# Kernel tuning notes

Hardware: AMD Instinct MI355X
Metric: run time of the kernel (lower is better)

## Reference

```python
import jax, jax.numpy as jnp
import numpy as np

N_NODES = 50000
N_EDGES = 800000


def _layer_norm(h, g, b, eps=1e-5):
    mu = jnp.mean(h, axis=-1, keepdims=True)
    var = jnp.var(h, axis=-1, keepdims=True)
    return (h - mu) * jax.lax.rsqrt(var + eps) * g + b


def _gat_layer(h, src, tgt, trans_prob, W, a_src, a_tgt, Wtp, a_tp, Wskip, b, concat):
    """GATLayerImp3-style edge-softmax attention with transition-prob scores."""
    N = h.shape[0]
    NH, F = a_src.shape
    proj = (h @ W).reshape(N, NH, F)                       # (N, NH, F)
    s_src = jnp.einsum('nhf,hf->nh', proj, a_src)          # (N, NH)
    s_tgt = jnp.einsum('nhf,hf->nh', proj, a_tgt)
    e = s_src[src] + s_tgt[tgt]                            # (E, NH)
    tp_proj = (trans_prob @ Wtp).reshape(-1, NH, F)        # (E, NH, F)
    e = e + jnp.einsum('ehf,hf->eh', tp_proj, a_tp)
    e = jax.nn.leaky_relu(e, 0.2)
    # neighborhood softmax over edges sharing the same target node
    m = jax.ops.segment_max(e, tgt, num_segments=N)        # (N, NH)
    w = jnp.exp(e - m[tgt])
    denom = jax.ops.segment_sum(w, tgt, num_segments=N)
    alpha = w / (denom[tgt] + 1e-16)                       # (E, NH)
    msg = proj[src] * alpha[..., None]                     # (E, NH, F)
    out = jax.ops.segment_sum(msg, tgt, num_segments=N)    # (N, NH, F)
    if Wskip is None:
        out = out + h[:, None, :]                          # F == F_in
    else:
        out = out + (h @ Wskip).reshape(N, NH, F)
    out = out.reshape(N, NH * F) if concat else out.mean(axis=1)
    return jax.nn.elu(out + b)


def setup_inputs() -> dict:
    key = jax.random.key(0)
    ks = jax.random.split(key, 32)
    s = 0.1
    inp = {
        'node_features': jax.random.normal(ks[0], (N_NODES, 128), jnp.float32),
        'edge_index': jax.random.randint(ks[1], (2, N_EDGES), 0, N_NODES, jnp.int32),
        'edge_prob': jax.random.uniform(ks[2], (N_EDGES, 1), jnp.float32),
        'x': jax.random.randint(ks[3], (64, 128), 0, N_NODES, jnp.int32),
        'W0': jax.random.normal(ks[4], (128, 256)) * s,
        'a_src0': jax.random.normal(ks[5], (16, 16)) * s,
        'a_tgt0': jax.random.normal(ks[6], (16, 16)) * s,
        'Wtp0': jax.random.normal(ks[7], (1, 256)) * s,
        'a_tp0': jax.random.normal(ks[8], (16, 16)) * s,
        'Wskip0': jax.random.normal(ks[9], (128, 256)) * s,
        'b0': jnp.zeros((256,)),
        'W1': jax.random.normal(ks[10], (256, 256)) * s,
        'a_src1': jax.random.normal(ks[11], (16, 16)) * s,
        'a_tgt1': jax.random.normal(ks[12], (16, 16)) * s,
        'Wtp1': jax.random.normal(ks[13], (1, 256)) * s,
        'a_tp1': jax.random.normal(ks[14], (16, 16)) * s,
        'Wskip1': jax.random.normal(ks[15], (256, 256)) * s,
        'b1': jnp.zeros((256,)),
        'ln1_g': jnp.ones((256,)),
        'ln1_b': jnp.zeros((256,)),
        'W2': jax.random.normal(ks[16], (256, 256)) * s,
        'a_src2': jax.random.normal(ks[17], (1, 256)) * s,
        'a_tgt2': jax.random.normal(ks[18], (1, 256)) * s,
        'Wtp2': jax.random.normal(ks[19], (1, 256)) * s,
        'a_tp2': jax.random.normal(ks[20], (1, 256)) * s,
        'b2': jnp.zeros((256,)),
        'ln2_g': jnp.ones((256,)),
        'ln2_b': jnp.zeros((256,)),
    }
    return inp


def reference(node_features, edge_index, edge_prob, x,
              W0, a_src0, a_tgt0, Wtp0, a_tp0, Wskip0, b0,
              W1, a_src1, a_tgt1, Wtp1, a_tp1, Wskip1, b1, ln1_g, ln1_b,
              W2, a_src2, a_tgt2, Wtp2, a_tp2, b2, ln2_g, ln2_b):
    src, tgt = edge_index[0], edge_index[1]
    # node encoder GAT layer (concat 16 heads x 16 feats -> 256)
    h = _gat_layer(node_features, src, tgt, edge_prob,
                   W0, a_src0, a_tgt0, Wtp0, a_tp0, Wskip0, b0, concat=True)
    # GM layer 0: GAT (concat) + layer norm
    h = _gat_layer(h, src, tgt, edge_prob,
                   W1, a_src1, a_tgt1, Wtp1, a_tp1, Wskip1, b1, concat=True)
    h = _layer_norm(h, ln1_g, ln1_b)
    # GM layer 1: GAT (avg last, 1 head x 256; skip is identity add) + layer norm
    h = _gat_layer(h, src, tgt, edge_prob,
                   W2, a_src2, a_tgt2, Wtp2, a_tp2, None, b2, concat=False)
    h = _layer_norm(h, ln2_g, ln2_b)
    # indexed gather of node embeddings into per-sequence embeddings
    out = h[x]                                              # (B, S, d_model)
    return out
```

## Files before the change

### kernel.cpp

```cpp
#include <hip/hip_runtime.h>
#include <hip/hip_fp16.h>
#include <math.h>

typedef __attribute__((ext_vector_type(8))) short    s16x8;
typedef __attribute__((ext_vector_type(8))) _Float16 h16x8;
typedef __attribute__((ext_vector_type(4))) float    f32x4;
typedef __attribute__((ext_vector_type(4))) int      i32x4;

__device__ __forceinline__ short f2h(float x){ return __half_as_short(__float2half(x)); }
__device__ __forceinline__ float h2f(short s){ return __half2float(__short_as_half(s)); }

__global__ void k_cvt(const float* __restrict__ in, short* __restrict__ outb, int n4){
  int i = blockIdx.x*blockDim.x + threadIdx.x;
  if (i >= n4) return;
  float4 v = ((const float4*)in)[i];
  short4 u; u.x = f2h(v.x); u.y = f2h(v.y); u.z = f2h(v.z); u.w = f2h(v.w);
  ((short4*)outb)[i] = u;
}

__global__ void k_prep(const float* W0, const float* Ws0, const float* W1,
                       const float* Ws1, const float* W2,
                       short* W0t, short* Ws0t, short* W1t, short* Ws1t, short* W2t,
                       const float* Wtp0, const float* a_tp0,
                       const float* Wtp1, const float* a_tp1,
                       const float* Wtp2, const float* a_tp2, float* cvec){
  __shared__ float buf[256];
  int b = blockIdx.x;
  if (b < 1024){
    int idx = b*256 + threadIdx.x;
    const float* W; short* Wt; int K; int base;
    if (idx < 32768)      { W=W0;  Wt=W0t;  K=128; base=0; }
    else if (idx < 65536) { W=Ws0; Wt=Ws0t; K=128; base=32768; }
    else if (idx < 131072){ W=W1;  Wt=W1t;  K=256; base=65536; }
    else if (idx < 196608){ W=Ws1; Wt=Ws1t; K=256; base=131072; }
    else                  { W=W2;  Wt=W2t;  K=256; base=196608; }
    int i = idx - base;
    int n = i / K, k = i - n*K;
    Wt[i] = f2h(W[(size_t)k*256 + n]);
  } else {
    int layer = b - 1024;
    const float* Wtp = layer==0 ? Wtp0 : (layer==1 ? Wtp1 : Wtp2);
    const float* atp = layer==0 ? a_tp0 : (layer==1 ? a_tp1 : a_tp2);
    float* c = cvec + (layer==0 ? 0 : (layer==1 ? 16 : 32));
    int NH = (layer==2) ? 1 : 16;
    int t = threadIdx.x;
    buf[t] = Wtp[t] * atp[t];
    __syncthreads();
    int F = 256 / NH;
    if (t < NH){
      float s = 0.f;
      for (int f = 0; f < F; f++) s += buf[t*F + f];
      c[t] = s;
    }
  }
}

__global__ void k_hist(const int* tgt, int* counts, int E){
  int i = blockIdx.x*blockDim.x + threadIdx.x;
  if (i < E) atomicAdd(&counts[tgt[i]], 1);
}
__global__ void k_scan1(const int* counts, int* row_excl, int* partials, int N){
  __shared__ int buf[1024];
  int t = threadIdx.x; int i = blockIdx.x*1024 + t;
  int v = (i < N) ? counts[i] : 0;
  buf[t] = v; __syncthreads();
  for (int o = 1; o < 1024; o <<= 1){
    int x = (t >= o) ? buf[t-o] : 0;
    __syncthreads();
    buf[t] += x;
    __syncthreads();
  }
  if (i < N) row_excl[i] = buf[t] - v;
  if (t == 1023) partials[blockIdx.x] = buf[1023];
}
__global__ void k_scan2(int* partials, int NB){
  if (threadIdx.x == 0 && blockIdx.x == 0){
    int s = 0;
    for (int b = 0; b < NB; b++){ int v = partials[b]; partials[b] = s; s += v; }
  }
}
__global__ void k_scan3(int* row_start, const int* partials, int* cursor, int N, int E){
  int i = blockIdx.x*blockDim.x + threadIdx.x;
  if (i < N){
    int v = row_start[i] + partials[i >> 10];
    row_start[i] = v; cursor[i] = v;
  }
  if (i == 0) row_start[N] = E;
}
__global__ void k_scatter(const int* src, const int* tgt, const float* eprob,
                          int* cursor, int2* es, int E){
  int i = blockIdx.x*blockDim.x + threadIdx.x;
  if (i >= E) return;
  int tg = tgt[i];
  int p = atomicAdd(&cursor[tg], 1);
  int2 v; v.x = src[i]; v.y = __float_as_int(eprob[i]);
  es[p] = v;
}

template<int KC>
__global__ __launch_bounds__(256)
void k_gemm_lds(const short* __restrict__ Ab,
                const short* __restrict__ B1t, const short* __restrict__ B2t,
                short* __restrict__ C1b, short* __restrict__ C2b,
                unsigned char* __restrict__ C8, float* __restrict__ pscale,
                const float* __restrict__ asrc, const float* __restrict__ atgt,
                const float* __restrict__ asrc1, const float* __restrict__ atgt1,
                float* __restrict__ s_src, float* __restrict__ s_tgt, int M){
  const int K = KC*32;
  __shared__ short lA[64*32];
  __shared__ short lB[256*32];
  const int tid  = threadIdx.x;
  const int lane = tid & 63;
  const int wave = tid >> 6;
  const int m16  = lane & 15;
  const int q    = lane >> 4;
  const int swz  = (m16 >> 1) & 3;
  const int r0   = blockIdx.x * 64;
  const bool first = (blockIdx.y == 0);
  const short* __restrict__ Bt = first ? B1t : B2t;
  short* __restrict__ Cb = first ? C1b : C2b;

  int arow = r0 + (tid >> 2); if (arow >= M) arow = M - 1;
  const int akq = (tid & 3) ^ ((tid >> 3) & 3);
  int bn[4], bkq[4];
  #pragma unroll
  for (int j = 0; j < 4; j++){
    int sj = j*256 + tid;
    bn[j]  = sj >> 2;
    bkq[j] = (sj & 3) ^ ((sj >> 3) & 3);
  }

  f32x4 acc[4][4];
  #pragma unroll
  for (int mi = 0; mi < 4; mi++)
    #pragma unroll
    for (int ni = 0; ni < 4; ni++) acc[mi][ni] = {0.f,0.f,0.f,0.f};

  s16x8 ra = *(const s16x8*)(Ab + (size_t)arow*K + akq*8);
  s16x8 rb[4];
  #pragma unroll
  for (int j = 0; j < 4; j++)
    rb[j] = *(const s16x8*)(Bt + (size_t)bn[j]*K + bkq[j]*8);

  for (int c = 0; c < KC; c++){
    __syncthreads();
    *(s16x8*)(lA + tid*8) = ra;
    #pragma unroll
    for (int j = 0; j < 4; j++)
      *(s16x8*)(lB + (j*256 + tid)*8) = rb[j];
    __syncthreads();

    if (c + 1 < KC){
      int k0 = (c+1)*32;
      ra = *(const s16x8*)(Ab + (size_t)arow*K + k0 + akq*8);
      #pragma unroll
      for (int j = 0; j < 4; j++)
        rb[j] = *(const s16x8*)(Bt + (size_t)bn[j]*K + k0 + bkq[j]*8);
    }

    s16x8 Af[4], Bf[4];
    #pragma unroll
    for (int mi = 0; mi < 4; mi++){
      int slot = (mi*16 + m16)*4 + (q ^ swz);
      Af[mi] = *(const s16x8*)(lA + slot*8);
    }
    #pragma unroll
    for (int ni = 0; ni < 4; ni++){
      int n = wave*64 + ni*16 + m16;
      int slot = n*4 + (q ^ swz);
      Bf[ni] = *(const s16x8*)(lB + slot*8);
    }
    #pragma unroll
    for (int mi = 0; mi < 4; mi++)
      #pragma unroll
      for (int ni = 0; ni < 4; ni++)
        acc[mi][ni] = __builtin_amdgcn_mfma_f32_16x16x32_f16(
            *(h16x8*)&Bf[ni], *(h16x8*)&Af[mi], acc[mi][ni], 0, 0, 0);
  }

  #pragma unroll
  for (int mi = 0; mi < 4; mi++){
    int row = r0 + mi*16 + m16;
    bool ok = (row < M);
    #pragma unroll
    for (int ni = 0; ni < 4; ni++){
      if (ok && Cb){
        size_t o = (size_t)row*256 + wave*64 + ni*16 + q*4;
        short4 u; u.x = f2h(acc[mi][ni][0]); u.y = f2h(acc[mi][ni][1]);
        u.z = f2h(acc[mi][ni][2]); u.w = f2h(acc[mi][ni][3]);
        *(short4*)(Cb + o) = u;
      }
      if (first && asrc){
        int hh = wave*4 + ni;
        const float* as = asrc + hh*16 + q*4;
        const float* at = atgt + hh*16 + q*4;
        float pss = acc[mi][ni][0]*as[0] + acc[mi][ni][1]*as[1]
                  + acc[mi][ni][2]*as[2] + acc[mi][ni][3]*as[3];
        float pst = acc[mi][ni][0]*at[0] + acc[mi][ni][1]*at[1]
                  + acc[mi][ni][2]*at[2] + acc[mi][ni][3]*at[3];
        pss += __shfl_xor(pss, 16); pss += __shfl_xor(pss, 32);
        pst += __shfl_xor(pst, 16); pst += __shfl_xor(pst, 32);
        if (ok && q == 0){
          s_src[row*16 + hh] = pss;
          s_tgt[row*16 + hh] = pst;
        }
      }
    }
  }

  if (first && asrc1){
    float pss[4], pst[4];
    #pragma unroll
    for (int mi = 0; mi < 4; mi++){
      float ss = 0.f, st = 0.f;
      #pragma unroll
      for (int ni = 0; ni < 4; ni++){
        const float* as = asrc1 + wave*64 + ni*16 + q*4;
        const float* at = atgt1 + wave*64 + ni*16 + q*4;
        #pragma unroll
        for (int k = 0; k < 4; k++){
          ss += acc[mi][ni][k]*as[k];
          st += acc[mi][ni][k]*at[k];
        }
      }
      ss += __shfl_xor(ss, 16); ss += __shfl_xor(ss, 32);
      st += __shfl_xor(st, 16); st += __shfl_xor(st, 32);
      pss[mi] = ss; pst[mi] = st;
    }
    __syncthreads();
    float* sred = (float*)lB;
    if (q == 0){
      #pragma unroll
      for (int mi = 0; mi < 4; mi++){
        int r = mi*16 + m16;
        sred[wave*64 + r]       = pss[mi];
        sred[256 + wave*64 + r] = pst[mi];
      }
    }
    __syncthreads();
    if (tid < 64){
      int row = r0 + tid;
      if (row < M){
        float ss = sred[tid] + sred[64+tid] + sred[128+tid] + sred[192+tid];
        float st = sred[256+tid] + sred[320+tid] + sred[384+tid] + sred[448+tid];
        s_src[row] = ss;
        s_tgt[row] = st;
      }
    }
  }

  if (first && C8){
    float am[4];
    #pragma unroll
    for (int mi = 0; mi < 4; mi++){
      float a = 0.f;
      #pragma unroll
      for (int ni = 0; ni < 4; ni++)
        #pragma unroll
        for (int k = 0; k < 4; k++)
          a = fmaxf(a, fabsf(acc[mi][ni][k]));
      a = fmaxf(a, __shfl_xor(a, 16));
      a = fmaxf(a, __shfl_xor(a, 32));
      am[mi] = a;
    }
    __syncthreads();
    float* rmax = (float*)lA;
    if (q == 0){
      #pragma unroll
      for (int mi = 0; mi < 4; mi++) rmax[wave*64 + mi*16 + m16] = am[mi];
    }
    __syncthreads();
    #pragma unroll
    for (int mi = 0; mi < 4; mi++){
      int r = mi*16 + m16;
      int row = r0 + r;
      bool ok = (row < M);
      float s = fmaxf(fmaxf(rmax[r], rmax[64+r]), fmaxf(rmax[128+r], rmax[192+r]));
      float scl = s * (1.f/127.f);
      float inv = (s > 0.f) ? (127.f/s) : 0.f;
      if (ok && wave == 0 && q == 0) pscale[row] = scl;
      if (ok){
        #pragma unroll
        for (int ni = 0; ni < 4; ni++){
          int v0 = __float2int_rn(acc[mi][ni][0]*inv) + 128;
          int v1 = __float2int_rn(acc[mi][ni][1]*inv) + 128;
          int v2 = __float2int_rn(acc[mi][ni][2]*inv) + 128;
          int v3 = __float2int_rn(acc[mi][ni][3]*inv) + 128;
          unsigned pk = (unsigned)(v0 & 255) | ((unsigned)(v1 & 255) << 8)
                      | ((unsigned)(v2 & 255) << 16) | ((unsigned)(v3 & 255) << 24);
          *(unsigned*)(C8 + (size_t)row*256 + wave*64 + ni*16 + q*4) = pk;
        }
      }
    }
  }
}

template<int LN>
__global__ __launch_bounds__(256)
void k_attn16(const int* __restrict__ row_start, const int2* __restrict__ es,
              const float* __restrict__ s_src, const float* __restrict__ s_tgt,
              const float* __restrict__ cvec,
              const unsigned char* __restrict__ proj8, const float* __restrict__ pscale,
              const short* __restrict__ skipb,
              const float* __restrict__ bias,
              const float* __restrict__ ln_g, const float* __restrict__ ln_b,
              short* __restrict__ houtb, int N){
  __shared__ __align__(16) float wbuf[4][16][20];
  __shared__ __align__(16) int   svbuf[4][16];
  __shared__ __align__(16) float scbuf[4][16];
  const int lane = threadIdx.x & 63;
  const int wave = threadIdx.x >> 6;
  const int node = blockIdx.x*4 + wave;
  if (node >= N) return;
  const int beg = row_start[node], end = row_start[node+1];

  const int h2 = lane >> 2;
  const int j4 = lane & 15;
  const int g  = lane >> 4;

  const f32x4 stg = *(const f32x4*)(s_tgt + (size_t)node*16 + g*4);
  const f32x4 cg  = *(const f32x4*)(cvec + g*4);

  float d = 0.f, dws = 0.f;
  float acc0 = 0.f, acc1 = 0.f, acc2 = 0.f, acc3 = 0.f;

  for (int s0 = beg; s0 < end; s0 += 16){
    int cnt = end - s0; if (cnt > 16) cnt = 16;
    int i  = s0 + j4;
    bool valid = (i < end);
    int ic = valid ? i : (end - 1);
    int2 e2 = es[ic];
    int sv = e2.x;
    float tp = __int_as_float(e2.y);
    f32x4 rv = *(const f32x4*)(s_src + (size_t)sv*16 + g*4);
    if (g == 0){ svbuf[wave][j4] = sv; scbuf[wave][j4] = pscale[sv]; }
    #pragma unroll
    for (int k = 0; k < 4; k++){
      float e = rv[k] + stg[k] + tp*cg[k];
      e = (e > 0.f) ? e : 0.2f*e;
      wbuf[wave][g*4 + k][j4] = valid ? __expf(e) : 0.f;
    }
    const unsigned* __restrict__ pp = (const unsigned*)proj8 + lane;
    for (int j = 0; j < cnt; j += 4){
      f32x4 w4  = *(const f32x4*)&wbuf[wave][h2][j];
      f32x4 sc4 = *(const f32x4*)&scbuf[wave][j];
      i32x4 sv4 = *(const i32x4*)&svbuf[wave][j];
      unsigned q0 = pp[(size_t)sv4.x*64];
      unsigned q1 = pp[(size_t)sv4.y*64];
      unsigned q2 = pp[(size_t)sv4.z*64];
      unsigned q3 = pp[(size_t)sv4.w*64];
      float ws0 = w4.x*sc4.x, ws1 = w4.y*sc4.y, ws2 = w4.z*sc4.z, ws3 = w4.w*sc4.w;
      d   += (w4.x + w4.y) + (w4.z + w4.w);
      dws += (ws0 + ws1) + (ws2 + ws3);
      acc0 += ws0*(float)(q0 & 255) + ws1*(float)(q1 & 255)
            + ws2*(float)(q2 & 255) + ws3*(float)(q3 & 255);
      acc1 += ws0*(float)((q0 >> 8) & 255) + ws1*(float)((q1 >> 8) & 255)
            + ws2*(float)((q2 >> 8) & 255) + ws3*(float)((q3 >> 8) & 255);
      acc2 += ws0*(float)((q0 >> 16) & 255) + ws1*(float)((q1 >> 16) & 255)
            + ws2*(float)((q2 >> 16) & 255) + ws3*(float)((q3 >> 16) & 255);
      acc3 += ws0*(float)(q0 >> 24) + ws1*(float)(q1 >> 24)
            + ws2*(float)(q2 >> 24) + ws3*(float)(q3 >> 24);
    }
  }
  float inv = 1.f / (d + 1e-16f);
  float c128 = 128.f * dws;

  short4 sk = ((const short4*)(skipb + (size_t)node*256))[lane];
  float acc[4];
  acc[0] = (acc0 - c128)*inv + h2f(sk.x); acc[1] = (acc1 - c128)*inv + h2f(sk.y);
  acc[2] = (acc2 - c128)*inv + h2f(sk.z); acc[3] = (acc3 - c128)*inv + h2f(sk.w);

  #pragma unroll
  for (int j = 0; j < 4; j++){
    float v = acc[j] + bias[lane*4 + j];
    acc[j] = (v > 0.f) ? v : (__expf(v) - 1.f);
  }
  if (LN){
    float s  = acc[0] + acc[1] + acc[2] + acc[3];
    float s2 = acc[0]*acc[0] + acc[1]*acc[1] + acc[2]*acc[2] + acc[3]*acc[3];
    for (int o = 32; o > 0; o >>= 1){ s += __shfl_xor(s, o); s2 += __shfl_xor(s2, o); }
    float mu  = s * (1.f/256.f);
    float var = s2 * (1.f/256.f) - mu*mu;
    float rs  = rsqrtf(var + 1e-5f);
    #pragma unroll
    for (int j = 0; j < 4; j++)
      acc[j] = (acc[j] - mu)*rs*ln_g[lane*4 + j] + ln_b[lane*4 + j];
  }
  short4 ub; ub.x = f2h(acc[0]); ub.y = f2h(acc[1]);
  ub.z = f2h(acc[2]); ub.w = f2h(acc[3]);
  ((short4*)(houtb + (size_t)node*256))[lane] = ub;
}

__global__ __launch_bounds__(256)
void k_attn1(const int* __restrict__ row_start, const int2* __restrict__ es,
             const float* __restrict__ s_src, const float* __restrict__ s_tgt,
             const float* __restrict__ cvec,
             const unsigned char* __restrict__ proj8, const float* __restrict__ pscale,
             const short* __restrict__ skipb,
             const float* __restrict__ bias,
             const float* __restrict__ ln_g, const float* __restrict__ ln_b,
             short* __restrict__ houtb, int N){
  __shared__ __align__(16) float wb1[4][64];
  __shared__ __align__(16) int   sb1[4][64];
  __shared__ __align__(16) float scb1[4][64];
  const int lane = threadIdx.x & 63;
  const int wave = threadIdx.x >> 6;
  const int node = blockIdx.x*4 + wave;
  if (node >= N) return;
  const int beg = row_start[node], end = row_start[node+1];

  const float c0 = cvec[0];
  const float st = s_tgt[node];
  float d = 0.f, dws = 0.f;
  float acc0 = 0.f, acc1 = 0.f, acc2 = 0.f, acc3 = 0.f;

  for (int s0 = beg; s0 < end; s0 += 64){
    int cnt = end - s0; if (cnt > 64) cnt = 64;
    int i  = s0 + lane;
    bool valid = (i < end);
    int ic = valid ? i : (end - 1);
    int2 e2 = es[ic];
    int sv = e2.x;
    float e = s_src[sv] + st + __int_as_float(e2.y)*c0;
    e = (e > 0.f) ? e : 0.2f*e;
    float w = valid ? __expf(e) : 0.f;
    wb1[wave][lane] = w;
    sb1[wave][lane] = sv;
    scb1[wave][lane] = pscale[sv];
    const unsigned* __restrict__ pp = (const unsigned*)proj8 + lane;
    for (int j = 0; j < cnt; j += 4){
      f32x4 w4  = *(const f32x4*)&wb1[wave][j];
      f32x4 sc4 = *(const f32x4*)&scb1[wave][j];
      i32x4 sv4 = *(const i32x4*)&sb1[wave][j];
      unsigned q0 = pp[(size_t)sv4.x*64];
      unsigned q1 = pp[(size_t)sv4.y*64];
      unsigned q2 = pp[(size_t)sv4.z*64];
      unsigned q3 = pp[(size_t)sv4.w*64];
      float ws0 = w4.x*sc4.x, ws1 = w4.y*sc4.y, ws2 = w4.z*sc4.z, ws3 = w4.w*sc4.w;
      d   += (w4.x + w4.y) + (w4.z + w4.w);
      dws += (ws0 + ws1) + (ws2 + ws3);
      acc0 += ws0*(float)(q0 & 255) + ws1*(float)(q1 & 255)
            + ws2*(float)(q2 & 255) + ws3*(float)(q3 & 255);
      acc1 += ws0*(float)((q0 >> 8) & 255) + ws1*(float)((q1 >> 8) & 255)
            + ws2*(float)((q2 >> 8) & 255) + ws3*(float)((q3 >> 8) & 255);
      acc2 += ws0*(float)((q0 >> 16) & 255) + ws1*(float)((q1 >> 16) & 255)
            + ws2*(float)((q2 >> 16) & 255) + ws3*(float)((q3 >> 16) & 255);
      acc3 += ws0*(float)(q0 >> 24) + ws1*(float)(q1 >> 24)
            + ws2*(float)(q2 >> 24) + ws3*(float)(q3 >> 24);
    }
  }
  float inv = 1.f / (d + 1e-16f);
  float c128 = 128.f * dws;

  short4 sk = ((const short4*)(skipb + (size_t)node*256))[lane];
  float acc[4];
  acc[0] = (acc0 - c128)*inv + h2f(sk.x); acc[1] = (acc1 - c128)*inv + h2f(sk.y);
  acc[2] = (acc2 - c128)*inv + h2f(sk.z); acc[3] = (acc3 - c128)*inv + h2f(sk.w);

  #pragma unroll
  for (int j = 0; j < 4; j++){
    float v = acc[j] + bias[lane*4 + j];
    acc[j] = (v > 0.f) ? v : (__expf(v) - 1.f);
  }
  float s  = acc[0] + acc[1] + acc[2] + acc[3];
  float s2 = acc[0]*acc[0] + acc[1]*acc[1] + acc[2]*acc[2] + acc[3]*acc[3];
  for (int o = 32; o > 0; o >>= 1){ s += __shfl_xor(s, o); s2 += __shfl_xor(s2, o); }
  float mu  = s * (1.f/256.f);
  float var = s2 * (1.f/256.f) - mu*mu;
  float rs  = rsqrtf(var + 1e-5f);
  #pragma unroll
  for (int j = 0; j < 4; j++)
    acc[j] = (acc[j] - mu)*rs*ln_g[lane*4 + j] + ln_b[lane*4 + j];
  short4 ub; ub.x = f2h(acc[0]); ub.y = f2h(acc[1]);
  ub.z = f2h(acc[2]); ub.w = f2h(acc[3]);
  ((short4*)(houtb + (size_t)node*256))[lane] = ub;
}

__global__ void k_gather(const short* hb, const int* x, float* out, int R){
  int r = blockIdx.x, t = threadIdx.x;
  if (r >= R) return;
  out[(size_t)r*256 + t] = h2f(hb[(size_t)x[r]*256 + t]);
}

extern "C" void kernel_launch(void* const* d_in, const int* in_sizes, int n_in,
                              void* d_out, int out_size, void* d_ws, size_t ws_size,
                              hipStream_t stream){
  const int N = in_sizes[0] / 128;
  const int E = in_sizes[1] / 2;
  const int R = in_sizes[3];

  const float* nf    = (const float*)d_in[0];
  const int*   ei    = (const int*)d_in[1];
  const float* eprob = (const float*)d_in[2];
  const int*   xidx  = (const int*)d_in[3];
  const float* W0     = (const float*)d_in[4];
  const float* a_src0 = (const float*)d_in[5];
  const float* a_tgt0 = (const float*)d_in[6];
  const float* Wtp0   = (const float*)d_in[7];
  const float* a_tp0  = (const float*)d_in[8];
  const float* Wskip0 = (const float*)d_in[9];
  const float* b0     = (const float*)d_in[10];
  const float* W1     = (const float*)d_in[11];
  const float* a_src1 = (const float*)d_in[12];
  const float* a_tgt1 = (const float*)d_in[13];
  const float* Wtp1   = (const float*)d_in[14];
  const float* a_tp1  = (const float*)d_in[15];
  const float* Wskip1 = (const float*)d_in[16];
  const float* b1     = (const float*)d_in[17];
  const float* ln1_g  = (const float*)d_in[18];
  const float* ln1_b  = (const float*)d_in[19];
  const float* W2     = (const float*)d_in[20];
  const float* a_src2 = (const float*)d_in[21];
  const float* a_tgt2 = (const float*)d_in[22];
  const float* Wtp2   = (const float*)d_in[23];
  const float* a_tp2  = (const float*)d_in[24];
  const float* b2     = (const float*)d_in[25];
  const float* ln2_g  = (const float*)d_in[26];
  const float* ln2_b  = (const float*)d_in[27];

  char* ws = (char*)d_ws;
  size_t off = 0;
  auto alloc = [&](size_t bytes)->char*{
    char* p = ws + off; off = (off + bytes + 255) & ~(size_t)255; return p;
  };
  unsigned char* P8 = (unsigned char*)alloc((size_t)N*256);
  float* pscale    = (float*)alloc((size_t)N*4);
  short* hXb       = (short*)alloc((size_t)N*256*2);
  short* Skb       = (short*)alloc((size_t)N*256*2);
  short* nfb       = (short*)alloc((size_t)N*128*2);
  float* s_src     = (float*)alloc((size_t)N*16*4);
  float* s_tgt     = (float*)alloc((size_t)N*16*4);
  float* cvec      = (float*)alloc(256);
  int*   counts    = (int*)alloc((size_t)N*4);
  int*   row_start = (int*)alloc((size_t)(N+1)*4);
  int*   partials  = (int*)alloc(256*4);
  int2*  es        = (int2*)alloc((size_t)E*8);
  short* W0t       = (short*)alloc((size_t)128*256*2);
  short* Ws0t      = (short*)alloc((size_t)128*256*2);
  short* W1t       = (short*)alloc((size_t)256*256*2);
  short* Ws1t      = (short*)alloc((size_t)256*256*2);
  short* W2t       = (short*)alloc((size_t)256*256*2);
  (void)ws_size; (void)n_in; (void)out_size;

  const int* src = ei;
  const int* tgt = ei + E;

  k_prep<<<1027, 256, 0, stream>>>(W0, Wskip0, W1, Wskip1, W2,
                                   W0t, Ws0t, W1t, Ws1t, W2t,
                                   Wtp0, a_tp0, Wtp1, a_tp1, Wtp2, a_tp2, cvec);
  k_cvt<<<((N*128/4)+255)/256, 256, 0, stream>>>(nf, nfb, N*128/4);
  hipMemsetAsync(counts, 0, (size_t)N*4, stream);

  k_hist<<<(E+255)/256, 256, 0, stream>>>(tgt, counts, E);
  int NB = (N + 1023) / 1024;
  k_scan1<<<NB, 1024, 0, stream>>>(counts, row_start, partials, N);
  k_scan2<<<1, 64, 0, stream>>>(partials, NB);
  k_scan3<<<(N+255)/256, 256, 0, stream>>>(row_start, partials, counts, N, E);
  k_scatter<<<(E+255)/256, 256, 0, stream>>>(src, tgt, eprob, counts, es, E);

  const int gt = (N + 63) / 64;
  const int at = (N + 3) / 4;

  k_gemm_lds<4><<<dim3(gt,2), 256, 0, stream>>>(nfb, W0t, Ws0t, nullptr, Skb, P8, pscale,
                                                a_src0, a_tgt0, nullptr, nullptr,
                                                s_src, s_tgt, N);
  k_attn16<0><<<at, 256, 0, stream>>>(row_start, es, s_src, s_tgt, cvec + 0,
                                      P8, pscale, Skb, b0, nullptr, nullptr, hXb, N);

  k_gemm_lds<8><<<dim3(gt,2), 256, 0, stream>>>(hXb, W1t, Ws1t, nullptr, Skb, P8, pscale,
                                                a_src1, a_tgt1, nullptr, nullptr,
                                                s_src, s_tgt, N);
  k_attn16<1><<<at, 256, 0, stream>>>(row_start, es, s_src, s_tgt, cvec + 16,
                                      P8, pscale, Skb, b1, ln1_g, ln1_b, hXb, N);

  k_gemm_lds<8><<<dim3(gt,1), 256, 0, stream>>>(hXb, W2t, nullptr, nullptr, nullptr,
                                                P8, pscale,
                                                nullptr, nullptr, a_src2, a_tgt2,
                                                s_src, s_tgt, N);
  k_attn1<<<at, 256, 0, stream>>>(row_start, es, s_src, s_tgt, cvec + 32,
                                  P8, pscale, hXb, b2, ln2_g, ln2_b, Skb, N);

  k_gather<<<R, 256, 0, stream>>>(Skb, xidx, (float*)d_out, R);
}
```

Baseline: 470.7 us.

## Cut preprocessing launches: fuse fp32 convert into GEMM, rank-based CSR scatter

Drops the separate fp32-to-fp16 conversion kernel; the first GEMM now loads fp32 node features and converts them on the fly. The counts memset is folded into the prep kernel. k_hist now records each edge's atomic rank, so the scatter computes positions as row_start plus rank instead of using a second atomic pass. The single-thread partial-scan kernel is removed: each scan3 block sums the preceding partials itself. Together these cut the number of launches and one full conversion pass, at the cost of an extra E-sized rank buffer and redundant per-block partial sums.

```diff
diff --git a/kernel.cpp b/kernel.cpp
--- a/kernel.cpp
+++ b/kernel.cpp
@@ -9,21 +9,14 @@
 
 __device__ __forceinline__ short f2h(float x){ return __half_as_short(__float2half(x)); }
 __device__ __forceinline__ float h2f(short s){ return __half2float(__short_as_half(s)); }
-
-__global__ void k_cvt(const float* __restrict__ in, short* __restrict__ outb, int n4){
-  int i = blockIdx.x*blockDim.x + threadIdx.x;
-  if (i >= n4) return;
-  float4 v = ((const float4*)in)[i];
-  short4 u; u.x = f2h(v.x); u.y = f2h(v.y); u.z = f2h(v.z); u.w = f2h(v.w);
-  ((short4*)outb)[i] = u;
-}
 
 __global__ void k_prep(const float* W0, const float* Ws0, const float* W1,
                        const float* Ws1, const float* W2,
                        short* W0t, short* Ws0t, short* W1t, short* Ws1t, short* W2t,
                        const float* Wtp0, const float* a_tp0,
                        const float* Wtp1, const float* a_tp1,
-                       const float* Wtp2, const float* a_tp2, float* cvec){
+                       const float* Wtp2, const float* a_tp2, float* cvec,
+                       int* counts, int N){
   __shared__ float buf[256];
   int b = blockIdx.x;
   if (b < 1024){
@@ -37,7 +30,7 @@
     int i = idx - base;
     int n = i / K, k = i - n*K;
     Wt[i] = f2h(W[(size_t)k*256 + n]);
-  } else {
+  } else if (b < 1027){
     int layer = b - 1024;
     const float* Wtp = layer==0 ? Wtp0 : (layer==1 ? Wtp1 : Wtp2);
     const float* atp = layer==0 ? a_tp0 : (layer==1 ? a_tp1 : a_tp2);
@@ -52,12 +45,15 @@
       for (int f = 0; f < F; f++) s += buf[t*F + f];
       c[t] = s;
     }
-  }
-}
-
-__global__ void k_hist(const int* tgt, int* counts, int E){
+  } else {
+    int i = (b - 1027)*256 + threadIdx.x;
+    if (i < N) counts[i] = 0;
+  }
+}
+
+__global__ void k_hist(const int* tgt, int* counts, int* rank, int E){
   int i = blockIdx.x*blockDim.x + threadIdx.x;
-  if (i < E) atomicAdd(&counts[tgt[i]], 1);
+  if (i < E) rank[i] = atomicAdd(&counts[tgt[i]], 1);
 }
 __global__ void k_scan1(const int* counts, int* row_excl, int* partials, int N){
   __shared__ int buf[1024];
@@ -73,33 +69,49 @@
   if (i < N) row_excl[i] = buf[t] - v;
   if (t == 1023) partials[blockIdx.x] = buf[1023];
 }
-__global__ void k_scan2(int* partials, int NB){
-  if (threadIdx.x == 0 && blockIdx.x == 0){
+__global__ void k_scan3(int* row_start, const int* partials, int N, int E){
+  __shared__ int base;
+  int b = blockIdx.x;
+  int pb = (b*256) >> 10;
+  if (threadIdx.x == 0){
     int s = 0;
-    for (int b = 0; b < NB; b++){ int v = partials[b]; partials[b] = s; s += v; }
-  }
-}
-__global__ void k_scan3(int* row_start, const int* partials, int* cursor, int N, int E){
-  int i = blockIdx.x*blockDim.x + threadIdx.x;
-  if (i < N){
-    int v = row_start[i] + partials[i >> 10];
-    row_start[i] = v; cursor[i] = v;
-  }
+    for (int k = 0; k < pb; k++) s += partials[k];
+    base = s;
+  }
+  __syncthreads();
+  int i = b*256 + threadIdx.x;
+  if (i < N) row_start[i] += base;
   if (i == 0) row_start[N] = E;
 }
 __global__ void k_scatter(const int* src, const int* tgt, const float* eprob,
-                          int* cursor, int2* es, int E){
+                          const int* row_start, const int* rank,
+                          long long* es, int E){
   int i = blockIdx.x*blockDim.x + threadIdx.x;
   if (i >= E) return;
-  int tg = tgt[i];
-  int p = atomicAdd(&cursor[tg], 1);
-  int2 v; v.x = src[i]; v.y = __float_as_int(eprob[i]);
-  es[p] = v;
-}
-
-template<int KC>
+  int p = row_start[tgt[i]] + rank[i];
+  unsigned long long v = ((unsigned long long)(unsigned)__float_as_int(eprob[i]) << 32)
+                       | (unsigned)src[i];
+  __builtin_nontemporal_store((long long)v, es + p);
+}
+
+template<int AF32>
+__device__ __forceinline__ s16x8 loadA(const void* Ab, size_t off){
+  if constexpr (AF32){
+    const float* p = (const float*)Ab + off;
+    float4 a0 = *(const float4*)p;
+    float4 a1 = *(const float4*)(p + 4);
+    s16x8 r;
+    r[0]=f2h(a0.x); r[1]=f2h(a0.y); r[2]=f2h(a0.z); r[3]=f2h(a0.w);
+    r[4]=f2h(a1.x); r[5]=f2h(a1.y); r[6]=f2h(a1.z); r[7]=f2h(a1.w);
+    return r;
+  } else {
+    return *(const s16x8*)((const short*)Ab + off);
+  }
+}
+
+template<int KC, int AF32>
 __global__ __launch_bounds__(256)
-void k_gemm_lds(const short* __restrict__ Ab,
+void k_gemm_lds(const void* __restrict__ Ab,
                 const short* __restrict__ B1t, const short* __restrict__ B2t,
                 short* __restrict__ C1b, short* __restrict__ C2b,
                 unsigned char* __restrict__ C8, float* __restrict__ pscale,
@@ -136,7 +148,7 @@
     #pragma unroll
     for (int ni = 0; ni < 4; ni++) acc[mi][ni] = {0.f,0.f,0.f,0.f};
 
-  s16x8 ra = *(const s16x8*)(Ab + (size_t)arow*K + akq*8);
+  s16x8 ra = loadA<AF32>(Ab, (size_t)arow*K + akq*8);
   s16x8 rb[4];
   #pragma unroll
   for (int j = 0; j < 4; j++)
@@ -152,7 +164,7 @@
 
     if (c + 1 < KC){
       int k0 = (c+1)*32;
-      ra = *(const s16x8*)(Ab + (size_t)arow*K + k0 + akq*8);
+      ra = loadA<AF32>(Ab, (size_t)arow*K + k0 + akq*8);
       #pragma unroll
       for (int j = 0; j < 4; j++)
         rb[j] = *(const s16x8*)(Bt + (size_t)bn[j]*K + k0 + bkq[j]*8);
@@ -527,13 +539,13 @@
   float* pscale    = (float*)alloc((size_t)N*4);
   short* hXb       = (short*)alloc((size_t)N*256*2);
   short* Skb       = (short*)alloc((size_t)N*256*2);
-  short* nfb       = (short*)alloc((size_t)N*128*2);
   float* s_src     = (float*)alloc((size_t)N*16*4);
   float* s_tgt     = (float*)alloc((size_t)N*16*4);
   float* cvec      = (float*)alloc(256);
   int*   counts    = (int*)alloc((size_t)N*4);
   int*   row_start = (int*)alloc((size_t)(N+1)*4);
   int*   partials  = (int*)alloc(256*4);
+  int*   rank      = (int*)alloc((size_t)E*4);
   int2*  es        = (int2*)alloc((size_t)E*8);
   short* W0t       = (short*)alloc((size_t)128*256*2);
   short* Ws0t      = (short*)alloc((size_t)128*256*2);
@@ -545,38 +557,38 @@
   const int* src = ei;
   const int* tgt = ei + E;
 
-  k_prep<<<1027, 256, 0, stream>>>(W0, Wskip0, W1, Wskip1, W2,
-                                   W0t, Ws0t, W1t, Ws1t, W2t,
-                                   Wtp0, a_tp0, Wtp1, a_tp1, Wtp2, a_tp2, cvec);
-  k_cvt<<<((N*128/4)+255)/256, 256, 0, stream>>>(nf, nfb, N*128/4);
-  hipMemsetAsync(counts, 0, (size_t)N*4, stream);
-
-  k_hist<<<(E+255)/256, 256, 0, stream>>>(tgt, counts, E);
+  int prep_blocks = 1027 + (N + 255)/256;
+  k_prep<<<prep_blocks, 256, 0, stream>>>(W0, Wskip0, W1, Wskip1, W2,
+                                          W0t, Ws0t, W1t, Ws1t, W2t,
+                                          Wtp0, a_tp0, Wtp1, a_tp1, Wtp2, a_tp2, cvec,
+                                          counts, N);
+
+  k_hist<<<(E+255)/256, 256, 0, stream>>>(tgt, counts, rank, E);
   int NB = (N + 1023) / 1024;
   k_scan1<<<NB, 1024, 0, stream>>>(counts, row_start, partials, N);
-  k_scan2<<<1, 64, 0, stream>>>(partials, NB);
-  k_scan3<<<(N+255)/256, 256, 0, stream>>>(row_start, partials, counts, N, E);
-  k_scatter<<<(E+255)/256, 256, 0, stream>>>(src, tgt, eprob, counts, es, E);
+  k_scan3<<<(N+255)/256, 256, 0, stream>>>(row_start, partials, N, E);
+  k_scatter<<<(E+255)/256, 256, 0, stream>>>(src, tgt, eprob, row_start, rank,
+                                             (long long*)es, E);
 
   const int gt = (N + 63) / 64;
   const int at = (N + 3) / 4;
 
-  k_gemm_lds<4><<<dim3(gt,2), 256, 0, stream>>>(nfb, W0t, Ws0t, nullptr, Skb, P8, pscale,
-                                                a_src0, a_tgt0, nullptr, nullptr,
-                                                s_src, s_tgt, N);
+  k_gemm_lds<4,1><<<dim3(gt,2), 256, 0, stream>>>(nf, W0t, Ws0t, nullptr, Skb, P8, pscale,
+                                                  a_src0, a_tgt0, nullptr, nullptr,
+                                                  s_src, s_tgt, N);
   k_attn16<0><<<at, 256, 0, stream>>>(row_start, es, s_src, s_tgt, cvec + 0,
                                       P8, pscale, Skb, b0, nullptr, nullptr, hXb, N);
 
-  k_gemm_lds<8><<<dim3(gt,2), 256, 0, stream>>>(hXb, W1t, Ws1t, nullptr, Skb, P8, pscale,
-                                                a_src1, a_tgt1, nullptr, nullptr,
-                                                s_src, s_tgt, N);
+  k_gemm_lds<8,0><<<dim3(gt,2), 256, 0, stream>>>(hXb, W1t, Ws1t, nullptr, Skb, P8, pscale,
+                                                  a_src1, a_tgt1, nullptr, nullptr,
+                                                  s_src, s_tgt, N);
   k_attn16<1><<<at, 256, 0, stream>>>(row_start, es, s_src, s_tgt, cvec + 16,
                                       P8, pscale, Skb, b1, ln1_g, ln1_b, hXb, N);
 
-  k_gemm_lds<8><<<dim3(gt,1), 256, 0, stream>>>(hXb, W2t, nullptr, nullptr, nullptr,
-                                                P8, pscale,
-                                                nullptr, nullptr, a_src2, a_tgt2,
-                                                s_src, s_tgt, N);
+  k_gemm_lds<8,0><<<dim3(gt,1), 256, 0, stream>>>(hXb, W2t, nullptr, nullptr, nullptr,
+                                                  P8, pscale,
+                                                  nullptr, nullptr, a_src2, a_tgt2,
+                                                  s_src, s_tgt, N);
   k_attn1<<<at, 256, 0, stream>>>(row_start, es, s_src, s_tgt, cvec + 32,
                                   P8, pscale, hXb, b2, ln2_g, ln2_b, Skb, N);
 
```

After: 443.8 us. 1.06x faster.
